# Kernel optimization log

Measured on AMD Instinct MI355X. Metric: run time of the kernel, lower is better.

Reference implementation:

```python
import jax, jax.numpy as jnp
import numpy as np

NUM_LAYERS = 3
EPS = 1e-12  # torch F.normalize eps

NU, NI, D = 200000, 100000, 64
E = 2000000
B = 8192


def setup_inputs() -> dict:
    key = jax.random.key(0)
    ks = jax.random.split(key, 7)
    # Xavier-uniform embeddings (fan_in = num_nodes, fan_out = D)
    def xavier(k, n, d):
        bound = np.sqrt(6.0 / (n + d))
        return jax.random.uniform(k, (n, d), jnp.float32, -bound, bound)
    return {
        "user_feat": xavier(ks[0], NU, D),
        "item_feat": xavier(ks[1], NI, D),
        "edge_u": jax.random.randint(ks[2], (E,), 0, NU, jnp.int32),
        "edge_i": jax.random.randint(ks[3], (E,), 0, NI, jnp.int32),
        "users": jax.random.randint(ks[4], (B,), 0, NU, jnp.int32),
        "pos_items": jax.random.randint(ks[5], (B,), 0, NI, jnp.int32),
        "neg_items": jax.random.randint(ks[6], (B,), 0, NI, jnp.int32),
    }


def _l2norm(h):
    n = jnp.sqrt(jnp.sum(h * h, axis=1, keepdims=True))
    return h / jnp.maximum(n, EPS)


def reference(user_feat, item_feat, edge_u, edge_i, users, pos_items, neg_items):
    Nu, Ni = user_feat.shape[0], item_feat.shape[0]
    ones = jnp.ones(edge_u.shape[0], jnp.float32)
    # symmetric degree norm, identical for both edge directions
    deg_u = jax.ops.segment_sum(ones, edge_u, num_segments=Nu)
    deg_i = jax.ops.segment_sum(ones, edge_i, num_segments=Ni)
    norm = (deg_u[edge_u] * deg_i[edge_i]) ** -0.5  # [E]
    norm = norm[:, None]  # [E,1]

    uh, ih = user_feat, item_feat
    ue, ie = user_feat, item_feat
    for k in range(NUM_LAYERS):
        # gather-scale-scatter for both edge directions using pre-layer feats
        new_ih = jax.ops.segment_sum(norm * uh[edge_u], edge_i, num_segments=Ni)
        new_uh = jax.ops.segment_sum(norm * ih[edge_i], edge_u, num_segments=Nu)
        uh, ih = _l2norm(new_uh), _l2norm(new_ih)
        ue = ue + uh * (1.0 / (k + 1))
        ie = ie + ih * (1.0 / (k + 1))

    return ue[users], ie[pos_items], ie[neg_items]
```

## Files before the change

kernel.cpp:

```cpp
#include <hip/hip_runtime.h>
#include <math.h>


__device__ __forceinline__ unsigned short f2bf(float f) {
    unsigned int b = __float_as_uint(f);
    b += 0x7FFFu + ((b >> 16) & 1u);
    return (unsigned short)(b >> 16);
}
__device__ __forceinline__ float bf2f(unsigned short u) {
    return __uint_as_float(((unsigned int)u) << 16);
}

__global__ void count_deg_kernel(const int* __restrict__ eu, const int* __restrict__ ei,
                                 int* __restrict__ deg, int E, int NU) {
    int e = blockIdx.x * blockDim.x + threadIdx.x;
    if (e >= E) return;
    atomicAdd(&deg[eu[e]], 1);
    atomicAdd(&deg[NU + ei[e]], 1);
}

__global__ void bump_kernel(const int* __restrict__ deg, int* __restrict__ offs,
                            int* __restrict__ cursor, float* __restrict__ isd,
                            int* __restrict__ total, int n) {
    int i = blockIdx.x * blockDim.x + threadIdx.x;
    if (i >= n) return;
    int d = deg[i];
    int o = atomicAdd(total, d);
    offs[i] = o;
    cursor[i] = o;
    isd[i] = d > 0 ? rsqrtf((float)d) : 0.f;
}

__global__ void conv_bf16_kernel(const float* __restrict__ src,
                                 unsigned short* __restrict__ dst, int n4) {
    int t = blockIdx.x * blockDim.x + threadIdx.x;
    if (t >= n4) return;
    float4 f = ((const float4*)src)[t];
    ushort4 o;
    o.x = f2bf(f.x); o.y = f2bf(f.y); o.z = f2bf(f.z); o.w = f2bf(f.w);
    ((ushort4*)dst)[t] = o;
}

__global__ void fill_csr_kernel(const int* __restrict__ eu, const int* __restrict__ ei,
                                const float* __restrict__ isd,
                                int* __restrict__ cursor, int2* __restrict__ csr,
                                int E, int NU) {
    int t = blockIdx.x * blockDim.x + threadIdx.x;
    if (t < E) {
        int u = eu[t], v = ei[t];
        float w = isd[u] * isd[NU + v];
        csr[atomicAdd(&cursor[u], 1)] = make_int2(v, __float_as_int(w));
    } else if (t < 2 * E) {
        int e = t - E;
        int u = eu[e], v = ei[e];
        float w = isd[u] * isd[NU + v];
        csr[atomicAdd(&cursor[NU + v], 1)] = make_int2(u, __float_as_int(w));
    }
}

__device__ __forceinline__ float4 gather16(const unsigned short* __restrict__ sfeat,
                                           const int2* __restrict__ csr,
                                           int start, int dcount, int l16) {
    float4 a0 = make_float4(0.f, 0.f, 0.f, 0.f);
    float4 a1 = make_float4(0.f, 0.f, 0.f, 0.f);
    float4 a2 = make_float4(0.f, 0.f, 0.f, 0.f);
    float4 a3 = make_float4(0.f, 0.f, 0.f, 0.f);
    int j = 0;
    for (; j + 3 < dcount; j += 4) {
        int2 e0 = csr[start + j];
        int2 e1 = csr[start + j + 1];
        int2 e2 = csr[start + j + 2];
        int2 e3 = csr[start + j + 3];
        ushort4 f0 = *(const ushort4*)(sfeat + (size_t)e0.x * 64 + l16 * 4);
        ushort4 f1 = *(const ushort4*)(sfeat + (size_t)e1.x * 64 + l16 * 4);
        ushort4 f2 = *(const ushort4*)(sfeat + (size_t)e2.x * 64 + l16 * 4);
        ushort4 f3 = *(const ushort4*)(sfeat + (size_t)e3.x * 64 + l16 * 4);
        float w0 = __int_as_float(e0.y), w1 = __int_as_float(e1.y);
        float w2 = __int_as_float(e2.y), w3 = __int_as_float(e3.y);
        a0.x = fmaf(w0, bf2f(f0.x), a0.x); a0.y = fmaf(w0, bf2f(f0.y), a0.y);
        a0.z = fmaf(w0, bf2f(f0.z), a0.z); a0.w = fmaf(w0, bf2f(f0.w), a0.w);
        a1.x = fmaf(w1, bf2f(f1.x), a1.x); a1.y = fmaf(w1, bf2f(f1.y), a1.y);
        a1.z = fmaf(w1, bf2f(f1.z), a1.z); a1.w = fmaf(w1, bf2f(f1.w), a1.w);
        a2.x = fmaf(w2, bf2f(f2.x), a2.x); a2.y = fmaf(w2, bf2f(f2.y), a2.y);
        a2.z = fmaf(w2, bf2f(f2.z), a2.z); a2.w = fmaf(w2, bf2f(f2.w), a2.w);
        a3.x = fmaf(w3, bf2f(f3.x), a3.x); a3.y = fmaf(w3, bf2f(f3.y), a3.y);
        a3.z = fmaf(w3, bf2f(f3.z), a3.z); a3.w = fmaf(w3, bf2f(f3.w), a3.w);
    }
    for (; j < dcount; ++j) {
        int2 e0 = csr[start + j];
        float w0 = __int_as_float(e0.y);
        ushort4 f0 = *(const ushort4*)(sfeat + (size_t)e0.x * 64 + l16 * 4);
        a0.x = fmaf(w0, bf2f(f0.x), a0.x); a0.y = fmaf(w0, bf2f(f0.y), a0.y);
        a0.z = fmaf(w0, bf2f(f0.z), a0.z); a0.w = fmaf(w0, bf2f(f0.w), a0.w);
    }
    float4 a = make_float4(a0.x + a1.x + a2.x + a3.x,
                           a0.y + a1.y + a2.y + a3.y,
                           a0.z + a1.z + a2.z + a3.z,
                           a0.w + a1.w + a2.w + a3.w);
    float ss = a.x * a.x + a.y * a.y + a.z * a.z + a.w * a.w;
    #pragma unroll
    for (int m = 1; m <= 8; m <<= 1) ss += __shfl_xor(ss, m, 64);
    float scale = 1.f / fmaxf(sqrtf(ss), 1e-12f);
    a.x *= scale; a.y *= scale; a.z *= scale; a.w *= scale;
    return a;
}

__global__ void prop_both_kernel(const unsigned short* __restrict__ uc,
                                 const unsigned short* __restrict__ ic,
                                 unsigned short* __restrict__ ud,
                                 unsigned short* __restrict__ id,
                                 const int* __restrict__ offs, const int* __restrict__ deg,
                                 const int2* __restrict__ csr, int NU, int NT) {
    int t = blockIdx.x * blockDim.x + threadIdx.x;
    int r = t >> 4;
    if (r >= NT) return;
    int l16 = t & 15;
    const unsigned short* sfeat;
    unsigned short* dst;
    if (r < NU) { sfeat = ic; dst = ud + (size_t)r * 64; }
    else        { sfeat = uc; dst = id + (size_t)(r - NU) * 64; }
    int start  = offs[r];
    int dcount = deg[r];
    float4 a = gather16(sfeat, csr, start, dcount, l16);
    ushort4 o;
    o.x = f2bf(a.x); o.y = f2bf(a.y); o.z = f2bf(a.z); o.w = f2bf(a.w);
    *(ushort4*)(dst + l16 * 4) = o;
}

__global__ void final_kernel(const float* __restrict__ user_feat,
                             const float* __restrict__ item_feat,
                             const unsigned short* __restrict__ uhA,
                             const unsigned short* __restrict__ ihA,
                             const unsigned short* __restrict__ uhB,
                             const unsigned short* __restrict__ ihB,
                             const int* __restrict__ users, const int* __restrict__ pos,
                             const int* __restrict__ neg,
                             const int* __restrict__ offs, const int* __restrict__ deg,
                             const int2* __restrict__ csr, float* __restrict__ out,
                             int NU, int B) {
    int t = blockIdx.x * blockDim.x + threadIdx.x;
    int s = t >> 4;
    if (s >= 3 * B) return;
    int l16 = t & 15;
    int seg = s / B, b = s - seg * B;
    int r, idx;
    const unsigned short *sfeat, *h1, *h2;
    const float* orig;
    if (seg == 0) {
        idx = users[b]; r = idx;
        sfeat = ihB; orig = user_feat; h1 = uhA; h2 = uhB;
    } else {
        idx = (seg == 1) ? pos[b] : neg[b];
        r = NU + idx;
        sfeat = uhB; orig = item_feat; h1 = ihA; h2 = ihB;
    }
    int start  = offs[r];
    int dcount = deg[r];
    float4 a = gather16(sfeat, csr, start, dcount, l16);
    float4 o = *(const float4*)(orig + (size_t)idx * 64 + l16 * 4);
    ushort4 v1 = *(const ushort4*)(h1 + (size_t)idx * 64 + l16 * 4);
    ushort4 v2 = *(const ushort4*)(h2 + (size_t)idx * 64 + l16 * 4);
    const float c3 = 1.0f / 3.0f;
    o.x += bf2f(v1.x) + 0.5f * bf2f(v2.x) + c3 * a.x;
    o.y += bf2f(v1.y) + 0.5f * bf2f(v2.y) + c3 * a.y;
    o.z += bf2f(v1.z) + 0.5f * bf2f(v2.z) + c3 * a.z;
    o.w += bf2f(v1.w) + 0.5f * bf2f(v2.w) + c3 * a.w;
    *(float4*)(out + (size_t)s * 64 + l16 * 4) = o;
}

extern "C" void kernel_launch(void* const* d_in, const int* in_sizes, int n_in,
                              void* d_out, int out_size, void* d_ws, size_t ws_size,
                              hipStream_t stream) {
    const float* user_feat = (const float*)d_in[0];
    const float* item_feat = (const float*)d_in[1];
    const int* edge_u = (const int*)d_in[2];
    const int* edge_i = (const int*)d_in[3];
    const int* users  = (const int*)d_in[4];
    const int* pos    = (const int*)d_in[5];
    const int* neg    = (const int*)d_in[6];
    float* out = (float*)d_out;

    const int D = 64;
    const int NU = in_sizes[0] / D;
    const int NI = in_sizes[1] / D;
    const int E  = in_sizes[2];
    const int B  = in_sizes[4];
    const int NT = NU + NI;

    char* ws = (char*)d_ws;
    size_t off = 0;
    auto alloc = [&](size_t bytes) -> void* {
        void* p = ws + off;
        off += bytes;
        off = (off + 255) & ~(size_t)255;
        return p;
    };
    size_t zbytes = (size_t)(NT + 1) * 4;
    char* zbase = (char*)alloc(zbytes);
    int* deg   = (int*)zbase;
    int* total = deg + NT;
    int*   offs   = (int*)alloc((size_t)NT * 4);
    int*   cursor = (int*)alloc((size_t)NT * 4);
    float* isd    = (float*)alloc((size_t)NT * 4);
    int2*  csr    = (int2*)alloc((size_t)2 * E * 8);
    unsigned short* ufb = (unsigned short*)alloc((size_t)NU * D * 2);
    unsigned short* ifb = (unsigned short*)alloc((size_t)NI * D * 2);
    unsigned short* uhA = (unsigned short*)alloc((size_t)NU * D * 2);
    unsigned short* ihA = (unsigned short*)alloc((size_t)NI * D * 2);
    unsigned short* uhB = (unsigned short*)alloc((size_t)NU * D * 2);
    unsigned short* ihB = (unsigned short*)alloc((size_t)NI * D * 2);

    hipMemsetAsync(zbase, 0, zbytes, stream);

    const int tb = 256;
    count_deg_kernel<<<(E + tb - 1) / tb, tb, 0, stream>>>(edge_u, edge_i, deg, E, NU);
    bump_kernel<<<(NT + tb - 1) / tb, tb, 0, stream>>>(deg, offs, cursor, isd, total, NT);

    int n4u = NU * D / 4, n4i = NI * D / 4;
    conv_bf16_kernel<<<(n4u + tb - 1) / tb, tb, 0, stream>>>(user_feat, ufb, n4u);
    conv_bf16_kernel<<<(n4i + tb - 1) / tb, tb, 0, stream>>>(item_feat, ifb, n4i);

    fill_csr_kernel<<<(2 * E + tb - 1) / tb, tb, 0, stream>>>(edge_u, edge_i, isd,
                                                              cursor, csr, E, NU);

    int pthreads = NT * 16;
    prop_both_kernel<<<(pthreads + tb - 1) / tb, tb, 0, stream>>>(
        ufb, ifb, uhA, ihA, offs, deg, csr, NU, NT);
    prop_both_kernel<<<(pthreads + tb - 1) / tb, tb, 0, stream>>>(
        uhA, ihA, uhB, ihB, offs, deg, csr, NU, NT);
    int fthreads = 3 * B * 16;
    final_kernel<<<(fthreads + tb - 1) / tb, tb, 0, stream>>>(
        user_feat, item_feat, uhA, ihA, uhB, ihB,
        users, pos, neg, offs, deg, csr, out, NU, B);
}
```

Measured before the change: 704.1 us.

## Partition CSR fill by output window per block group; deepen gather unroll

The CSR fill kernel now runs as a fixed grid split into 8 block groups. Each group handles only the edges whose destination row offset falls in one eighth of the CSR array, so concurrently resident blocks scatter into a smaller address window, aiming for better write locality. In exchange, every group reads all edges, offsets and indices, roughly 8x the input reads. Separately, the gather loop now issues 8 feature loads before accumulating, for more loads in flight, but uses a single accumulator instead of four.

```diff
diff --git a/kernel.cpp b/kernel.cpp
--- a/kernel.cpp
+++ b/kernel.cpp
@@ -43,66 +43,62 @@
 
 __global__ void fill_csr_kernel(const int* __restrict__ eu, const int* __restrict__ ei,
                                 const float* __restrict__ isd,
+                                const int* __restrict__ offs,
                                 int* __restrict__ cursor, int2* __restrict__ csr,
-                                int E, int NU) {
-    int t = blockIdx.x * blockDim.x + threadIdx.x;
-    if (t < E) {
-        int u = eu[t], v = ei[t];
+                                int E, int NU, int shift) {
+    int g   = blockIdx.x & 7;
+    int gb  = blockIdx.x >> 3;
+    int nbg = gridDim.x >> 3;
+    int tg  = gb * blockDim.x + threadIdx.x;
+    int TG  = nbg * blockDim.x;
+    int tot = 2 * E;
+    for (int t = tg; t < tot; t += TG) {
+        int e = (t < E) ? t : t - E;
+        int u = eu[e], v = ei[e];
+        int row = (t < E) ? u : NU + v;
+        int o = offs[row];
+        if (((o >> shift) & 7) != g) continue;
         float w = isd[u] * isd[NU + v];
-        csr[atomicAdd(&cursor[u], 1)] = make_int2(v, __float_as_int(w));
-    } else if (t < 2 * E) {
-        int e = t - E;
-        int u = eu[e], v = ei[e];
-        float w = isd[u] * isd[NU + v];
-        csr[atomicAdd(&cursor[NU + v], 1)] = make_int2(u, __float_as_int(w));
+        int src = (t < E) ? v : u;
+        csr[atomicAdd(&cursor[row], 1)] = make_int2(src, __float_as_int(w));
     }
 }
 
 __device__ __forceinline__ float4 gather16(const unsigned short* __restrict__ sfeat,
                                            const int2* __restrict__ csr,
                                            int start, int dcount, int l16) {
-    float4 a0 = make_float4(0.f, 0.f, 0.f, 0.f);
-    float4 a1 = make_float4(0.f, 0.f, 0.f, 0.f);
-    float4 a2 = make_float4(0.f, 0.f, 0.f, 0.f);
-    float4 a3 = make_float4(0.f, 0.f, 0.f, 0.f);
+    float4 acc = make_float4(0.f, 0.f, 0.f, 0.f);
     int j = 0;
-    for (; j + 3 < dcount; j += 4) {
-        int2 e0 = csr[start + j];
-        int2 e1 = csr[start + j + 1];
-        int2 e2 = csr[start + j + 2];
-        int2 e3 = csr[start + j + 3];
-        ushort4 f0 = *(const ushort4*)(sfeat + (size_t)e0.x * 64 + l16 * 4);
-        ushort4 f1 = *(const ushort4*)(sfeat + (size_t)e1.x * 64 + l16 * 4);
-        ushort4 f2 = *(const ushort4*)(sfeat + (size_t)e2.x * 64 + l16 * 4);
-        ushort4 f3 = *(const ushort4*)(sfeat + (size_t)e3.x * 64 + l16 * 4);
-        float w0 = __int_as_float(e0.y), w1 = __int_as_float(e1.y);
-        float w2 = __int_as_float(e2.y), w3 = __int_as_float(e3.y);
-        a0.x = fmaf(w0, bf2f(f0.x), a0.x); a0.y = fmaf(w0, bf2f(f0.y), a0.y);
-        a0.z = fmaf(w0, bf2f(f0.z), a0.z); a0.w = fmaf(w0, bf2f(f0.w), a0.w);
-        a1.x = fmaf(w1, bf2f(f1.x), a1.x); a1.y = fmaf(w1, bf2f(f1.y), a1.y);
-        a1.z = fmaf(w1, bf2f(f1.z), a1.z); a1.w = fmaf(w1, bf2f(f1.w), a1.w);
-        a2.x = fmaf(w2, bf2f(f2.x), a2.x); a2.y = fmaf(w2, bf2f(f2.y), a2.y);
-        a2.z = fmaf(w2, bf2f(f2.z), a2.z); a2.w = fmaf(w2, bf2f(f2.w), a2.w);
-        a3.x = fmaf(w3, bf2f(f3.x), a3.x); a3.y = fmaf(w3, bf2f(f3.y), a3.y);
-        a3.z = fmaf(w3, bf2f(f3.z), a3.z); a3.w = fmaf(w3, bf2f(f3.w), a3.w);
+    for (; j + 7 < dcount; j += 8) {
+        int2 eb[8];
+        #pragma unroll
+        for (int k = 0; k < 8; ++k) eb[k] = csr[start + j + k];
+        ushort4 fb[8];
+        #pragma unroll
+        for (int k = 0; k < 8; ++k)
+            fb[k] = *(const ushort4*)(sfeat + (size_t)eb[k].x * 64 + l16 * 4);
+        #pragma unroll
+        for (int k = 0; k < 8; ++k) {
+            float w = __int_as_float(eb[k].y);
+            acc.x = fmaf(w, bf2f(fb[k].x), acc.x);
+            acc.y = fmaf(w, bf2f(fb[k].y), acc.y);
+            acc.z = fmaf(w, bf2f(fb[k].z), acc.z);
+            acc.w = fmaf(w, bf2f(fb[k].w), acc.w);
+        }
     }
     for (; j < dcount; ++j) {
         int2 e0 = csr[start + j];
         float w0 = __int_as_float(e0.y);
         ushort4 f0 = *(const ushort4*)(sfeat + (size_t)e0.x * 64 + l16 * 4);
-        a0.x = fmaf(w0, bf2f(f0.x), a0.x); a0.y = fmaf(w0, bf2f(f0.y), a0.y);
-        a0.z = fmaf(w0, bf2f(f0.z), a0.z); a0.w = fmaf(w0, bf2f(f0.w), a0.w);
-    }
-    float4 a = make_float4(a0.x + a1.x + a2.x + a3.x,
-                           a0.y + a1.y + a2.y + a3.y,
-                           a0.z + a1.z + a2.z + a3.z,
-                           a0.w + a1.w + a2.w + a3.w);
-    float ss = a.x * a.x + a.y * a.y + a.z * a.z + a.w * a.w;
+        acc.x = fmaf(w0, bf2f(f0.x), acc.x); acc.y = fmaf(w0, bf2f(f0.y), acc.y);
+        acc.z = fmaf(w0, bf2f(f0.z), acc.z); acc.w = fmaf(w0, bf2f(f0.w), acc.w);
+    }
+    float ss = acc.x * acc.x + acc.y * acc.y + acc.z * acc.z + acc.w * acc.w;
     #pragma unroll
     for (int m = 1; m <= 8; m <<= 1) ss += __shfl_xor(ss, m, 64);
     float scale = 1.f / fmaxf(sqrtf(ss), 1e-12f);
-    a.x *= scale; a.y *= scale; a.z *= scale; a.w *= scale;
-    return a;
+    acc.x *= scale; acc.y *= scale; acc.z *= scale; acc.w *= scale;
+    return acc;
 }
 
 __global__ void prop_both_kernel(const unsigned short* __restrict__ uc,
@@ -220,8 +216,12 @@
     conv_bf16_kernel<<<(n4u + tb - 1) / tb, tb, 0, stream>>>(user_feat, ufb, n4u);
     conv_bf16_kernel<<<(n4i + tb - 1) / tb, tb, 0, stream>>>(item_feat, ifb, n4i);
 
-    fill_csr_kernel<<<(2 * E + tb - 1) / tb, tb, 0, stream>>>(edge_u, edge_i, isd,
-                                                              cursor, csr, E, NU);
+    int slots = 2 * E;
+    int per_win = (slots + 7) / 8;
+    int shift = 0;
+    while ((1 << shift) < per_win) ++shift;
+    fill_csr_kernel<<<2048, tb, 0, stream>>>(edge_u, edge_i, isd, offs,
+                                             cursor, csr, E, NU, shift);
 
     int pthreads = NT * 16;
     prop_both_kernel<<<(pthreads + tb - 1) / tb, tb, 0, stream>>>(
```

Result: slower. 828.7 us (+17.7%).
